# Kernel optimization log

Hardware: AMD Instinct MI355X
Metric: run time of the kernel (lower is better)

Reference implementation:

```python
import jax, jax.numpy as jnp
import numpy as np
import math

B, S, E, H = 2, 2048, 1024, 16


def setup_inputs() -> dict:
    key = jax.random.key(0)
    ks = jax.random.split(key, 9)
    std = 0.02
    return {
        "x": jax.random.normal(ks[0], (B, S, E), dtype=jnp.float32),
        "Wq": jax.random.normal(ks[1], (E, E), dtype=jnp.float32) * std,
        "bq": jnp.zeros((E,), dtype=jnp.float32),
        "Wk": jax.random.normal(ks[2], (E, E), dtype=jnp.float32) * std,
        "bk": jnp.zeros((E,), dtype=jnp.float32),
        "Wv": jax.random.normal(ks[3], (E, E), dtype=jnp.float32) * std,
        "bv": jnp.zeros((E,), dtype=jnp.float32),
        "Wfc": jax.random.normal(ks[4], (E, E), dtype=jnp.float32) * std,
        "bfc": jnp.zeros((E,), dtype=jnp.float32),
        "n_head": H,
    }


def reference(x, Wq, bq, Wk, bk, Wv, bv, Wfc, bfc, n_head):
    Bn, Sn, En = x.shape
    Hd = En // n_head  # head_dim
    # torch Linear: y = x @ W.T + b
    def proj(W, b):
        return (x @ W.T + b).reshape(Bn, Sn, n_head, Hd).transpose(0, 2, 1, 3)  # [B,H,S,D]
    q = proj(Wq, bq)
    k = proj(Wk, bk)
    v = proj(Wv, bv)
    scores = jnp.einsum('bhqd,bhkd->bhqk', q, k) / math.sqrt(Hd)  # [B,H,S,S]
    # ALiBi: slopes_h = 2^{-(h+1)}; alibi[h,i,j] = -slope_h * (i - j)
    slopes = 2.0 ** (-jnp.arange(1, n_head + 1, dtype=jnp.float32))  # [H]
    pos = jnp.arange(Sn, dtype=jnp.float32)
    rel = pos[:, None] - pos[None, :]  # [S,S], memory_pos - context_pos
    alibi = -slopes[:, None, None] * rel  # [H,S,S]
    scores = scores + alibi[None]
    weights = jax.nn.softmax(scores, axis=-1)  # [B,H,S,S]
    out = jnp.einsum('bhqk,bhkd->bqhd', weights, v).reshape(Bn, Sn, En)
    out = out @ Wfc.T + bfc
    return (out, weights)
```

## Files before the change

kernel.cpp:

```cpp
#include <hip/hip_runtime.h>
#include <hip/hip_bf16.h>
#include <cstdint>
#include <cstddef>

#define BB 2
#define SS 2048
#define EE 1024
#define HH 16
#define MM (BB*SS)

typedef __bf16 bf16;
typedef __bf16 bf16x8 __attribute__((ext_vector_type(8)));
typedef float f32x4 __attribute__((ext_vector_type(4)));

#define GLD16(gsrc, ldst) \
  __builtin_amdgcn_global_load_lds((const __attribute__((address_space(1))) void*)(gsrc), \
                                   (__attribute__((address_space(3))) void*)(ldst), 16, 0, 0)

__global__ __launch_bounds__(256) void cvt_f32_bf16(const float* __restrict__ src,
                                                    bf16* __restrict__ dst, int n) {
    int i = (blockIdx.x * 256 + threadIdx.x) * 8;
    if (i >= n) return;
    float4 a = *(const float4*)(src + i);
    float4 b = *(const float4*)(src + i + 4);
    bf16 o[8] = {(bf16)a.x,(bf16)a.y,(bf16)a.z,(bf16)a.w,
                 (bf16)b.x,(bf16)b.y,(bf16)b.z,(bf16)b.w};
    *(uint4*)(dst + i) = *(uint4*)o;
}

__global__ __launch_bounds__(256) void cvt4(const float* __restrict__ a, const float* __restrict__ b,
                                            const float* __restrict__ c, const float* __restrict__ d,
                                            bf16* __restrict__ oa, bf16* __restrict__ ob,
                                            bf16* __restrict__ oc, bf16* __restrict__ od) {
    int sel = blockIdx.y;
    const float* s = sel == 0 ? a : sel == 1 ? b : sel == 2 ? c : d;
    bf16* o       = sel == 0 ? oa : sel == 1 ? ob : sel == 2 ? oc : od;
    int i = (blockIdx.x * 256 + threadIdx.x) * 8;
    float4 x = *(const float4*)(s + i);
    float4 y = *(const float4*)(s + i + 4);
    bf16 t[8] = {(bf16)x.x,(bf16)x.y,(bf16)x.z,(bf16)x.w,
                 (bf16)y.x,(bf16)y.y,(bf16)y.z,(bf16)y.w};
    *(uint4*)(o + i) = *(uint4*)t;
}

template<int MODE>
__global__ __launch_bounds__(256) void gemm128(const bf16* __restrict__ A,
                                               const bf16* __restrict__ W0,
                                               const bf16* __restrict__ W1,
                                               const bf16* __restrict__ W2,
                                               const float* __restrict__ b0,
                                               const float* __restrict__ b1,
                                               const float* __restrict__ b2,
                                               void* __restrict__ o0,
                                               void* __restrict__ o1,
                                               void* __restrict__ o2) {
    __shared__ bf16 Al[128*64];
    __shared__ bf16 Bl[128*64];
    const int t = threadIdx.x;
    const int wsel = blockIdx.x >> 3;
    const int n0 = (blockIdx.x & 7) * 128;
    const int m0 = blockIdx.y * 128;
    const bf16* W  = wsel == 0 ? W0 : wsel == 1 ? W1 : W2;
    const float* bias = wsel == 0 ? b0 : wsel == 1 ? b1 : b2;
    void* outp = wsel == 0 ? o0 : wsel == 1 ? o1 : o2;

    const int w = t >> 6, lane = t & 63, lg = lane >> 4, li = lane & 15;
    const int wr = w >> 1, wc = w & 1;
    f32x4 acc[4][4] = {};

    for (int k0 = 0; k0 < 1024; k0 += 64) {
        __syncthreads();
        #pragma unroll
        for (int i = 0; i < 4; ++i) {
            int f = i * 256 + t;
            int row = f >> 3, c = (f & 7) * 8;
            GLD16(A + (size_t)(m0 + row) * 1024 + k0 + c, Al + f * 8);
            GLD16(W + (size_t)(n0 + row) * 1024 + k0 + c, Bl + f * 8);
        }
        __syncthreads();
        #pragma unroll
        for (int ks = 0; ks < 2; ++ks) {
            bf16x8 af[4], bf_[4];
            #pragma unroll
            for (int m = 0; m < 4; ++m)
                af[m] = *(const bf16x8*)&Al[(wr*64 + m*16 + li)*64 + ks*32 + lg*8];
            #pragma unroll
            for (int n = 0; n < 4; ++n)
                bf_[n] = *(const bf16x8*)&Bl[(wc*64 + n*16 + li)*64 + ks*32 + lg*8];
            #pragma unroll
            for (int m = 0; m < 4; ++m)
                #pragma unroll
                for (int n = 0; n < 4; ++n)
                    acc[m][n] = __builtin_amdgcn_mfma_f32_16x16x32_bf16(af[m], bf_[n], acc[m][n], 0,0,0);
        }
    }
    #pragma unroll
    for (int m = 0; m < 4; ++m)
      #pragma unroll
      for (int n = 0; n < 4; ++n)
        #pragma unroll
        for (int r = 0; r < 4; ++r) {
            int row = m0 + wr*64 + m*16 + lg*4 + r;
            int col = n0 + wc*64 + n*16 + li;
            float v = acc[m][n][r] + bias[col];
            if (MODE == 0) {
                int b = row >> 11, s = row & (SS-1);
                int h = col >> 6, d = col & 63;
                ((bf16*)outp)[(((size_t)(b*HH + h)*SS + s) << 6) + d] = (bf16)v;
            } else {
                ((float*)outp)[(size_t)row*1024 + col] = v;
            }
        }
}

__global__ __launch_bounds__(256) void transpose_v(const bf16* __restrict__ V,
                                                   bf16* __restrict__ Vt) {
    __shared__ bf16 L[64][72];
    const int bh = blockIdx.y, s0 = blockIdx.x * 64, t = threadIdx.x;
    for (int id = t; id < 512; id += 256) {
        int row = id >> 3, c = id & 7;
        *(uint4*)&L[row][c*8] = *(const uint4*)&V[((size_t)bh*SS + s0 + row)*64 + c*8];
    }
    __syncthreads();
    for (int id = t; id < 512; id += 256) {
        int d = id >> 3, c = id & 7;
        bf16 tmp[8];
        #pragma unroll
        for (int jj = 0; jj < 8; ++jj) tmp[jj] = L[c*8 + jj][d];
        *(uint4*)&Vt[((size_t)bh*64 + d)*SS + s0 + c*8] = *(uint4*)tmp;
    }
}

__global__ __launch_bounds__(256) void lsum_kernel(const bf16* __restrict__ Q,
                                                   const bf16* __restrict__ Kk,
                                                   float* __restrict__ Lpart) {
    __shared__ bf16 ring[2][64*64];
    __shared__ float Lred[2][64];

    const int lin = blockIdx.x + (int)(gridDim.x * blockIdx.y);
    const int nl  = (lin & 7) * 256 + (lin >> 3);
    const int bh = nl >> 6, rr = nl & 63;
    const int qt = rr >> 1, jh2 = rr & 1;

    const int h = bh & 15;
    const int q0 = qt * 64;
    const int jbase = jh2 * 1024;
    const int t = threadIdx.x, w = t >> 6, lane = t & 63, lg = lane >> 4, li = lane & 15;
    const int jh = w & 1, qh = w >> 1;
    const float slope = exp2f(-(float)(h + 1));
    const size_t kvbase = (size_t)bh * SS * 64;
    const float L2E = 1.4426950408889634f;
    const float K1 = 0.125f * L2E;
    const float C  = slope * L2E;
    const float C64 = C * 64.f;

    bf16x8 aq[2][2];
    #pragma unroll
    for (int cbq = 0; cbq < 2; ++cbq) {
        const bf16* qptr = Q + kvbase + (size_t)(q0 + qh*32 + cbq*16 + li) * 64;
        aq[cbq][0] = *(const bf16x8*)(qptr + lg*8);
        aq[cbq][1] = *(const bf16x8*)(qptr + 32 + lg*8);
    }
    const int swz = (li & 7) << 4;

    #define STAGE_K(J0, DST) do {                                              \
        _Pragma("unroll")                                                      \
        for (int i_ = 0; i_ < 2; ++i_) {                                       \
            int f_ = i_*256 + t; int row_ = f_ >> 3, c_ = f_ & 7;              \
            GLD16(Kk + kvbase + (size_t)((J0) + row_)*64 + (c_ ^ (row_ & 7))*8,\
                  (DST) + f_*8);                                               \
        } } while (0)

    float cj[2][4];
    #pragma unroll
    for (int jt = 0; jt < 2; ++jt)
        #pragma unroll
        for (int r = 0; r < 4; ++r)
            cj[jt][r] = C * (float)(jbase + jh*32 + jt*16 + lg*4 + r - (SS-1));
    float lp[2] = {0.f, 0.f};

    STAGE_K(jbase, &ring[0][0]);
    __syncthreads();
    for (int kt = 0; kt < 16; ++kt) {
        const int cur = kt & 1;
        if (kt + 1 < 16) STAGE_K(jbase + (kt+1)*64, &ring[cur ^ 1][0]);
        const char* Ksb = (const char*)&ring[cur][0];
        bf16x8 ak[2][2];
        #pragma unroll
        for (int jt = 0; jt < 2; ++jt) {
            int row = jh*32 + jt*16 + li;
            ak[jt][0] = *(const bf16x8*)(Ksb + row*128 + ((     lg*16) ^ swz));
            ak[jt][1] = *(const bf16x8*)(Ksb + row*128 + ((64 + lg*16) ^ swz));
        }
        f32x4 sc[2][2] = {};
        __builtin_amdgcn_s_setprio(1);
        #pragma unroll
        for (int jt = 0; jt < 2; ++jt)
            #pragma unroll
            for (int cbq = 0; cbq < 2; ++cbq) {
                sc[jt][cbq] = __builtin_amdgcn_mfma_f32_16x16x32_bf16(ak[jt][0], aq[cbq][0], sc[jt][cbq], 0,0,0);
                sc[jt][cbq] = __builtin_amdgcn_mfma_f32_16x16x32_bf16(ak[jt][1], aq[cbq][1], sc[jt][cbq], 0,0,0);
            }
        __builtin_amdgcn_s_setprio(0);
        #pragma unroll
        for (int jt = 0; jt < 2; ++jt) {
            #pragma unroll
            for (int cbq = 0; cbq < 2; ++cbq)
                #pragma unroll
                for (int r = 0; r < 4; ++r)
                    lp[cbq] += __builtin_amdgcn_exp2f(fmaf(sc[jt][cbq][r], K1, cj[jt][r]));
            #pragma unroll
            for (int r = 0; r < 4; ++r) cj[jt][r] += C64;
        }
        __syncthreads();
    }
    #pragma unroll
    for (int cbq = 0; cbq < 2; ++cbq) {
        lp[cbq] += __shfl_xor(lp[cbq], 16);
        lp[cbq] += __shfl_xor(lp[cbq], 32);
    }
    if (lg == 0) {
        Lred[jh][qh*32 + li]      = lp[0];
        Lred[jh][qh*32 + 16 + li] = lp[1];
    }
    __syncthreads();
    if (t < 64)
        Lpart[((size_t)(jh2*32 + bh))*SS + q0 + t] = Lred[0][t] + Lred[1][t];
    #undef STAGE_K
}

__global__ __launch_bounds__(1024) void lfix_kernel(const float* __restrict__ Lpart,
                                                    float* __restrict__ Lbuf) {
    int i = blockIdx.x * 1024 + threadIdx.x;
    Lbuf[i] = __builtin_amdgcn_logf(Lpart[i] + Lpart[65536 + i]);
}

__global__ __launch_bounds__(256) void wpv_kernel(const bf16* __restrict__ Q,
                                                  const bf16* __restrict__ Kk,
                                                  const bf16* __restrict__ Vt,
                                                  const float* __restrict__ Lbuf,
                                                  float* __restrict__ wout,
                                                  bf16* __restrict__ opart0,
                                                  bf16* __restrict__ opart1) {
    __shared__ bf16 ring[4][64*64];

    const int lin = blockIdx.x + (int)(gridDim.x * blockIdx.y);
    const int nl  = (lin & 7) * 256 + (lin >> 3);
    const int bh = nl >> 6, rr = nl & 63;
    const int qt = rr >> 1, jh2 = rr & 1;

    const int b = bh >> 4, h = bh & 15;
    const int q0 = qt * 64;
    const int jbase = jh2 * 1024;
    const int t = threadIdx.x, w = t >> 6, lane = t & 63, lg = lane >> 4, li = lane & 15;
    const int jh = w & 1, qh = w >> 1;
    const float slope = exp2f(-(float)(h + 1));
    const size_t kvbase = (size_t)bh * SS * 64;
    const size_t vtbase = (size_t)bh * 64 * SS;
    const float L2E = 1.4426950408889634f;
    const float K1 = 0.125f * L2E;
    const float C  = slope * L2E;
    const float C64 = C * 64.f;
    bf16* opart = jh2 == 0 ? opart0 : opart1;

    bf16x8 aq[2][2];
    float lgl[2];
    #pragma unroll
    for (int cbq = 0; cbq < 2; ++cbq) {
        const int qi = q0 + qh*32 + cbq*16 + li;
        const bf16* qptr = Q + kvbase + (size_t)qi * 64;
        aq[cbq][0] = *(const bf16x8*)(qptr + lg*8);
        aq[cbq][1] = *(const bf16x8*)(qptr + 32 + lg*8);
        lgl[cbq] = Lbuf[(size_t)bh*SS + qi];
    }
    const int swz = (li & 7) << 4;

    #define STAGE_K(J0, DST) do {                                              \
        _Pragma("unroll")                                                      \
        for (int i_ = 0; i_ < 2; ++i_) {                                       \
            int f_ = i_*256 + t; int row_ = f_ >> 3, c_ = f_ & 7;              \
            GLD16(Kk + kvbase + (size_t)((J0) + row_)*64 + (c_ ^ (row_ & 7))*8,\
                  (DST) + f_*8);                                               \
        } } while (0)
    #define STAGE_V(J0, DST) do {                                              \
        _Pragma("unroll")                                                      \
        for (int i_ = 0; i_ < 2; ++i_) {                                       \
            int f_ = i_*256 + t; int row_ = f_ >> 3, c_ = f_ & 7;              \
            GLD16(Vt + vtbase + (size_t)row_*SS + (J0) + (c_ ^ (row_ & 7))*8,  \
                  (DST) + f_*8);                                               \
        } } while (0)

    float ecr[2][2][4];
    #pragma unroll
    for (int jt = 0; jt < 2; ++jt)
        #pragma unroll
        for (int cbq = 0; cbq < 2; ++cbq)
            #pragma unroll
            for (int r = 0; r < 4; ++r)
                ecr[jt][cbq][r] = C * (float)(jbase + jh*32 + jt*16 + lg*4 + r - (SS-1)) - lgl[cbq];

    f32x4 acc[2][4] = {};
    float* wrow0 = wout + ((size_t)bh*SS + q0 + qh*32 +      li) * SS;
    float* wrow1 = wout + ((size_t)bh*SS + q0 + qh*32 + 16 + li) * SS;

    STAGE_K(jbase, &ring[0][0]);
    STAGE_V(jbase, &ring[2][0]);
    __syncthreads();
    for (int kt = 0; kt < 16; ++kt) {
        const int cur = kt & 1;
        const int j0 = jbase + kt * 64;
        if (kt + 1 < 16) {
            STAGE_K(j0 + 64, &ring[cur ^ 1][0]);
            STAGE_V(j0 + 64, &ring[2 + (cur ^ 1)][0]);
        }
        const char* Ksb = (const char*)&ring[cur][0];
        const char* Vsb = (const char*)&ring[2 + cur][0];
        bf16x8 ak[2][2];
        #pragma unroll
        for (int jt = 0; jt < 2; ++jt) {
            int row = jh*32 + jt*16 + li;
            ak[jt][0] = *(const bf16x8*)(Ksb + row*128 + ((     lg*16) ^ swz));
            ak[jt][1] = *(const bf16x8*)(Ksb + row*128 + ((64 + lg*16) ^ swz));
        }
        f32x4 sc[2][2] = {};
        __builtin_amdgcn_s_setprio(1);
        #pragma unroll
        for (int jt = 0; jt < 2; ++jt)
            #pragma unroll
            for (int cbq = 0; cbq < 2; ++cbq) {
                sc[jt][cbq] = __builtin_amdgcn_mfma_f32_16x16x32_bf16(ak[jt][0], aq[cbq][0], sc[jt][cbq], 0,0,0);
                sc[jt][cbq] = __builtin_amdgcn_mfma_f32_16x16x32_bf16(ak[jt][1], aq[cbq][1], sc[jt][cbq], 0,0,0);
            }
        __builtin_amdgcn_s_setprio(0);
        f32x4 wv[2][2];
        #pragma unroll
        for (int jt = 0; jt < 2; ++jt)
            #pragma unroll
            for (int cbq = 0; cbq < 2; ++cbq) {
                f32x4 v;
                v[0] = __builtin_amdgcn_exp2f(fmaf(sc[jt][cbq][0], K1, ecr[jt][cbq][0]));
                v[1] = __builtin_amdgcn_exp2f(fmaf(sc[jt][cbq][1], K1, ecr[jt][cbq][1]));
                v[2] = __builtin_amdgcn_exp2f(fmaf(sc[jt][cbq][2], K1, ecr[jt][cbq][2]));
                v[3] = __builtin_amdgcn_exp2f(fmaf(sc[jt][cbq][3], K1, ecr[jt][cbq][3]));
                wv[jt][cbq] = v;
                float* wr = (cbq == 0 ? wrow0 : wrow1);
                __builtin_nontemporal_store(v, (f32x4*)&wr[j0 + jh*32 + jt*16 + lg*4]);
                ecr[jt][cbq][0] += C64; ecr[jt][cbq][1] += C64;
                ecr[jt][cbq][2] += C64; ecr[jt][cbq][3] += C64;
            }
        bf16x8 pa[2];
        #pragma unroll
        for (int cbq = 0; cbq < 2; ++cbq) {
            bf16x8 p;
            p[0] = (bf16)wv[0][cbq][0]; p[1] = (bf16)wv[0][cbq][1];
            p[2] = (bf16)wv[0][cbq][2]; p[3] = (bf16)wv[0][cbq][3];
            p[4] = (bf16)wv[1][cbq][0]; p[5] = (bf16)wv[1][cbq][1];
            p[6] = (bf16)wv[1][cbq][2]; p[7] = (bf16)wv[1][cbq][3];
            pa[cbq] = p;
        }
        bf16x8 vb[4];
        #pragma unroll
        for (int d0 = 0; d0 < 4; ++d0) {
            int row = d0*16 + li;
            uint2 u0 = *(const uint2*)(Vsb + row*128 + ((jh*64      + lg*8) ^ swz));
            uint2 u1 = *(const uint2*)(Vsb + row*128 + ((jh*64 + 32 + lg*8) ^ swz));
            uint4 uu = {u0.x, u0.y, u1.x, u1.y};
            vb[d0] = __builtin_bit_cast(bf16x8, uu);
        }
        __builtin_amdgcn_s_setprio(1);
        #pragma unroll
        for (int cbq = 0; cbq < 2; ++cbq)
            #pragma unroll
            for (int d0 = 0; d0 < 4; ++d0)
                acc[cbq][d0] = __builtin_amdgcn_mfma_f32_16x16x32_bf16(pa[cbq], vb[d0], acc[cbq][d0], 0,0,0);
        __builtin_amdgcn_s_setprio(0);
        __syncthreads();
    }

    bf16* Obuf = &ring[0][0];
    #pragma unroll
    for (int cbq = 0; cbq < 2; ++cbq)
        #pragma unroll
        for (int d0 = 0; d0 < 4; ++d0)
            #pragma unroll
            for (int r = 0; r < 4; ++r)
                Obuf[jh*4096 + (qh*32 + cbq*16 + lg*4 + r)*64 + d0*16 + li] =
                    (bf16)acc[cbq][d0][r];
    __syncthreads();
    {
        int q = t >> 2, dc = (t & 3) << 4;
        const bf16* o0 = Obuf +        q*64 + dc;
        const bf16* o1 = Obuf + 4096 + q*64 + dc;
        bf16x8 a0 = *(const bf16x8*)(o0),     a1 = *(const bf16x8*)(o0 + 8);
        bf16x8 b0 = *(const bf16x8*)(o1),     b1 = *(const bf16x8*)(o1 + 8);
        bf16 ov[16];
        #pragma unroll
        for (int e = 0; e < 8; ++e) {
            ov[e]     = (bf16)((float)a0[e] + (float)b0[e]);
            ov[8 + e] = (bf16)((float)a1[e] + (float)b1[e]);
        }
        bf16* dst = opart + ((size_t)(b*SS + q0 + q))*EE + h*64 + dc;
        *(uint4*)(dst)     = *(uint4*)(ov);
        *(uint4*)(dst + 8) = *(uint4*)(ov + 8);
    }
    #undef STAGE_K
    #undef STAGE_V
}

__global__ __launch_bounds__(256) void ored_kernel(const bf16* __restrict__ O0,
                                                   const bf16* __restrict__ O1,
                                                   bf16* __restrict__ Ab) {
    int i = (blockIdx.x * 256 + threadIdx.x) * 8;
    bf16x8 a = *(const bf16x8*)(O0 + i);
    bf16x8 b = *(const bf16x8*)(O1 + i);
    bf16 o[8];
    #pragma unroll
    for (int e = 0; e < 8; ++e) o[e] = (bf16)((float)a[e] + (float)b[e]);
    *(uint4*)(Ab + i) = *(uint4*)o;
}

extern "C" void kernel_launch(void* const* d_in, const int* in_sizes, int n_in,
                              void* d_out, int out_size, void* d_ws, size_t ws_size,
                              hipStream_t stream) {
    const float* x   = (const float*)d_in[0];
    const float* Wq  = (const float*)d_in[1];
    const float* bq  = (const float*)d_in[2];
    const float* Wk  = (const float*)d_in[3];
    const float* bk  = (const float*)d_in[4];
    const float* Wv  = (const float*)d_in[5];
    const float* bv  = (const float*)d_in[6];
    const float* Wfc = (const float*)d_in[7];
    const float* bfc = (const float*)d_in[8];

    char* ws = (char*)d_ws;
    const size_t MB = 1024u*1024u;
    bf16* xb   = (bf16*)(ws + 0);
    bf16* wqb  = (bf16*)(ws + 8*MB);
    bf16* wkb  = (bf16*)(ws + 10*MB);
    bf16* wvb  = (bf16*)(ws + 12*MB);
    bf16* wfb  = (bf16*)(ws + 14*MB);
    bf16* Qb   = (bf16*)(ws + 16*MB);
    bf16* Kb   = (bf16*)(ws + 24*MB);
    bf16* Vb   = (bf16*)(ws + 32*MB);
    bf16* Vtb  = (bf16*)(ws + 40*MB);
    bf16* Ab   = (bf16*)(ws + 48*MB);
    bf16* Opart0 = (bf16*)(ws + 0);
    bf16* Opart1 = (bf16*)(ws + 32*MB);
    float* Lpart = (float*)(ws + 8*MB);
    float* Lb    = (float*)(ws + 9*MB);

    float* outp = (float*)d_out;
    float* wout = outp + (size_t)BB*SS*EE;

    cvt_f32_bf16<<<dim3(4194304/8/256), 256, 0, stream>>>(x, xb, 4194304);
    cvt4<<<dim3(512, 4), 256, 0, stream>>>(Wq, Wk, Wv, Wfc, wqb, wkb, wvb, wfb);

    gemm128<0><<<dim3(24, 32), 256, 0, stream>>>(xb, wqb, wkb, wvb, bq, bk, bv, Qb, Kb, Vb);

    transpose_v<<<dim3(SS/64, BB*HH), 256, 0, stream>>>(Vb, Vtb);

    lsum_kernel<<<dim3(64, 32), 256, 0, stream>>>(Qb, Kb, Lpart);
    lfix_kernel<<<dim3(64), 1024, 0, stream>>>(Lpart, Lb);

    wpv_kernel<<<dim3(64, 32), 256, 0, stream>>>(Qb, Kb, Vtb, Lb, wout, Opart0, Opart1);

    ored_kernel<<<dim3(2048), 256, 0, stream>>>(Opart0, Opart1, Ab);

    gemm128<1><<<dim3(8, 32), 256, 0, stream>>>(Ab, wfb, wfb, wfb, bfc, bfc, bfc, d_out, d_out, d_out);
}
```

Baseline: 319.8 us.

## Split weight-writing and PV accumulation into interleaved block roles of one kernel

The attention kernel now launches a 1D grid where four of every five blocks compute 128x128 score tiles and write the softmax weights to global memory. The fifth block of each group runs the original PV loop, which recomputes the probabilities only to feed the MFMA accumulation and no longer stores weights. This separates the store-bound weight output from the compute-bound PV pass so the two can overlap on different CUs. The cost is computing QK^T and exp twice, and the weight stores are no longer nontemporal.

```diff
diff --git a/kernel.cpp b/kernel.cpp
--- a/kernel.cpp
+++ b/kernel.cpp
@@ -235,33 +235,94 @@
     Lbuf[i] = __builtin_amdgcn_logf(Lpart[i] + Lpart[65536 + i]);
 }
 
-__global__ __launch_bounds__(256) void wpv_kernel(const bf16* __restrict__ Q,
+__global__ __launch_bounds__(256) void fat_kernel(const bf16* __restrict__ Q,
                                                   const bf16* __restrict__ Kk,
                                                   const bf16* __restrict__ Vt,
                                                   const float* __restrict__ Lbuf,
                                                   float* __restrict__ wout,
                                                   bf16* __restrict__ opart0,
                                                   bf16* __restrict__ opart1) {
-    __shared__ bf16 ring[4][64*64];
-
-    const int lin = blockIdx.x + (int)(gridDim.x * blockIdx.y);
-    const int nl  = (lin & 7) * 256 + (lin >> 3);
+    __shared__ bf16 lds[4][64*64];
+    const int id = blockIdx.x;
+    const int t = threadIdx.x, w = t >> 6, lane = t & 63, lg = lane >> 4, li = lane & 15;
+    const float L2E = 1.4426950408889634f;
+    const float K1 = 0.125f * L2E;
+    const int swz = (li & 7) << 4;
+
+    if (id % 5 != 4) {
+        const int wi = (id / 5) * 4 + (id % 5);
+        const int bh = wi >> 8, tile = wi & 255;
+        const int q0 = (tile >> 4) * 128, j0 = (tile & 15) * 128;
+        const int h = bh & 15;
+        const float slope = exp2f(-(float)(h + 1));
+        const float C = slope * L2E;
+        const size_t kvbase = (size_t)bh * SS * 64;
+        const int wj = w & 1, wq = w >> 1;
+
+        bf16* Qt = &lds[0][0];
+        bf16* Kt = &lds[2][0];
+        #pragma unroll
+        for (int i = 0; i < 4; ++i) {
+            int f = i * 256 + t; int row = f >> 3, c16 = f & 7;
+            GLD16(Q  + kvbase + (size_t)(q0 + row)*64 + (c16 ^ (row & 7))*8, Qt + f*8);
+            GLD16(Kk + kvbase + (size_t)(j0 + row)*64 + (c16 ^ (row & 7))*8, Kt + f*8);
+        }
+        __syncthreads();
+
+        const char* Qtb = (const char*)Qt;
+        const char* Ktb = (const char*)Kt;
+        bf16x8 aq[4][2];
+        float lgl[4];
+        #pragma unroll
+        for (int qt = 0; qt < 4; ++qt) {
+            int rl = wq*64 + qt*16 + li;
+            aq[qt][0] = *(const bf16x8*)(Qtb + rl*128 + ((     lg*16) ^ swz));
+            aq[qt][1] = *(const bf16x8*)(Qtb + rl*128 + ((64 + lg*16) ^ swz));
+            lgl[qt] = Lbuf[(size_t)bh*SS + q0 + rl];
+        }
+        #pragma unroll
+        for (int jt = 0; jt < 4; ++jt) {
+            int rl = wj*64 + jt*16 + li;
+            bf16x8 ak0 = *(const bf16x8*)(Ktb + rl*128 + ((     lg*16) ^ swz));
+            bf16x8 ak1 = *(const bf16x8*)(Ktb + rl*128 + ((64 + lg*16) ^ swz));
+            f32x4 sc[4] = {};
+            __builtin_amdgcn_s_setprio(1);
+            #pragma unroll
+            for (int qt = 0; qt < 4; ++qt) {
+                sc[qt] = __builtin_amdgcn_mfma_f32_16x16x32_bf16(ak0, aq[qt][0], sc[qt], 0,0,0);
+                sc[qt] = __builtin_amdgcn_mfma_f32_16x16x32_bf16(ak1, aq[qt][1], sc[qt], 0,0,0);
+            }
+            __builtin_amdgcn_s_setprio(0);
+            const float cjb = C * (float)(j0 + wj*64 + jt*16 + lg*4 - (SS-1));
+            #pragma unroll
+            for (int qt = 0; qt < 4; ++qt) {
+                f32x4 v;
+                v[0] = __builtin_amdgcn_exp2f(fmaf(sc[qt][0], K1, cjb           - lgl[qt]));
+                v[1] = __builtin_amdgcn_exp2f(fmaf(sc[qt][1], K1, cjb + C       - lgl[qt]));
+                v[2] = __builtin_amdgcn_exp2f(fmaf(sc[qt][2], K1, cjb + C*2.f   - lgl[qt]));
+                v[3] = __builtin_amdgcn_exp2f(fmaf(sc[qt][3], K1, cjb + C*3.f   - lgl[qt]));
+                float* wr_ = wout + ((size_t)bh*SS + q0 + wq*64 + qt*16 + li) * SS
+                                  + j0 + wj*64 + jt*16 + lg*4;
+                *(f32x4*)wr_ = v;
+            }
+        }
+        return;
+    }
+
+    const int nl = id / 5;
     const int bh = nl >> 6, rr = nl & 63;
     const int qt = rr >> 1, jh2 = rr & 1;
-
     const int b = bh >> 4, h = bh & 15;
     const int q0 = qt * 64;
     const int jbase = jh2 * 1024;
-    const int t = threadIdx.x, w = t >> 6, lane = t & 63, lg = lane >> 4, li = lane & 15;
     const int jh = w & 1, qh = w >> 1;
     const float slope = exp2f(-(float)(h + 1));
     const size_t kvbase = (size_t)bh * SS * 64;
     const size_t vtbase = (size_t)bh * 64 * SS;
-    const float L2E = 1.4426950408889634f;
-    const float K1 = 0.125f * L2E;
     const float C  = slope * L2E;
     const float C64 = C * 64.f;
     bf16* opart = jh2 == 0 ? opart0 : opart1;
+    bf16 (*ring)[64*64] = lds;
 
     bf16x8 aq[2][2];
     float lgl[2];
@@ -273,7 +334,6 @@
         aq[cbq][1] = *(const bf16x8*)(qptr + 32 + lg*8);
         lgl[cbq] = Lbuf[(size_t)bh*SS + qi];
     }
-    const int swz = (li & 7) << 4;
 
     #define STAGE_K(J0, DST) do {                                              \
         _Pragma("unroll")                                                      \
@@ -300,8 +360,6 @@
                 ecr[jt][cbq][r] = C * (float)(jbase + jh*32 + jt*16 + lg*4 + r - (SS-1)) - lgl[cbq];
 
     f32x4 acc[2][4] = {};
-    float* wrow0 = wout + ((size_t)bh*SS + q0 + qh*32 +      li) * SS;
-    float* wrow1 = wout + ((size_t)bh*SS + q0 + qh*32 + 16 + li) * SS;
 
     STAGE_K(jbase, &ring[0][0]);
     STAGE_V(jbase, &ring[2][0]);
@@ -332,32 +390,26 @@
                 sc[jt][cbq] = __builtin_amdgcn_mfma_f32_16x16x32_bf16(ak[jt][1], aq[cbq][1], sc[jt][cbq], 0,0,0);
             }
         __builtin_amdgcn_s_setprio(0);
-        f32x4 wv[2][2];
+        bf16x8 pa[2];
+        #pragma unroll
+        for (int cbq = 0; cbq < 2; ++cbq) {
+            bf16x8 p;
+            #pragma unroll
+            for (int jt = 0; jt < 2; ++jt) {
+                p[jt*4+0] = (bf16)__builtin_amdgcn_exp2f(fmaf(sc[jt][cbq][0], K1, ecr[jt][cbq][0]));
+                p[jt*4+1] = (bf16)__builtin_amdgcn_exp2f(fmaf(sc[jt][cbq][1], K1, ecr[jt][cbq][1]));
+                p[jt*4+2] = (bf16)__builtin_amdgcn_exp2f(fmaf(sc[jt][cbq][2], K1, ecr[jt][cbq][2]));
+                p[jt*4+3] = (bf16)__builtin_amdgcn_exp2f(fmaf(sc[jt][cbq][3], K1, ecr[jt][cbq][3]));
+            }
+            pa[cbq] = p;
+        }
         #pragma unroll
         for (int jt = 0; jt < 2; ++jt)
             #pragma unroll
             for (int cbq = 0; cbq < 2; ++cbq) {
-                f32x4 v;
-                v[0] = __builtin_amdgcn_exp2f(fmaf(sc[jt][cbq][0], K1, ecr[jt][cbq][0]));
-                v[1] = __builtin_amdgcn_exp2f(fmaf(sc[jt][cbq][1], K1, ecr[jt][cbq][1]));
-                v[2] = __builtin_amdgcn_exp2f(fmaf(sc[jt][cbq][2], K1, ecr[jt][cbq][2]));
-                v[3] = __builtin_amdgcn_exp2f(fmaf(sc[jt][cbq][3], K1, ecr[jt][cbq][3]));
-                wv[jt][cbq] = v;
-                float* wr = (cbq == 0 ? wrow0 : wrow1);
-                __builtin_nontemporal_store(v, (f32x4*)&wr[j0 + jh*32 + jt*16 + lg*4]);
                 ecr[jt][cbq][0] += C64; ecr[jt][cbq][1] += C64;
                 ecr[jt][cbq][2] += C64; ecr[jt][cbq][3] += C64;
             }
-        bf16x8 pa[2];
-        #pragma unroll
-        for (int cbq = 0; cbq < 2; ++cbq) {
-            bf16x8 p;
-            p[0] = (bf16)wv[0][cbq][0]; p[1] = (bf16)wv[0][cbq][1];
-            p[2] = (bf16)wv[0][cbq][2]; p[3] = (bf16)wv[0][cbq][3];
-            p[4] = (bf16)wv[1][cbq][0]; p[5] = (bf16)wv[1][cbq][1];
-            p[6] = (bf16)wv[1][cbq][2]; p[7] = (bf16)wv[1][cbq][3];
-            pa[cbq] = p;
-        }
         bf16x8 vb[4];
         #pragma unroll
         for (int d0 = 0; d0 < 4; ++d0) {
@@ -462,7 +514,7 @@
     lsum_kernel<<<dim3(64, 32), 256, 0, stream>>>(Qb, Kb, Lpart);
     lfix_kernel<<<dim3(64), 1024, 0, stream>>>(Lpart, Lb);
 
-    wpv_kernel<<<dim3(64, 32), 256, 0, stream>>>(Qb, Kb, Vtb, Lb, wout, Opart0, Opart1);
+    fat_kernel<<<dim3(10240), 256, 0, stream>>>(Qb, Kb, Vtb, Lb, wout, Opart0, Opart1);
 
     ored_kernel<<<dim3(2048), 256, 0, stream>>>(Opart0, Opart1, Ab);
 
```

After: 326.2 us. 1.02x slower.
